# Optimization experiments

Measured on AMD Instinct MI355X. Metric: run time of the kernel, lower is better.

The kernel has to match this reference:

```python
import jax, jax.numpy as jnp
from jax import lax
import numpy as np

D_STATE = 16
D_CONV = 4
GROUPS = 4
TOKEN = 8


def group_norm(x, w, b, groups, eps=1e-5):
    # x: [B, C, H, W]; torch GroupNorm semantics
    B, C, H, W = x.shape
    xg = x.reshape(B, groups, C // groups, H, W)
    mu = xg.mean(axis=(2, 3, 4), keepdims=True)
    var = ((xg - mu) ** 2).mean(axis=(2, 3, 4), keepdims=True)
    xg = (xg - mu) / jnp.sqrt(var + eps)
    return xg.reshape(B, C, H, W) * w[None, :, None, None] + b[None, :, None, None]


def mamba_fwd(x, in_w, conv_w, conv_b, xproj_w, dt_w, dt_b, A_log, D, out_w):
    # x: [B, L, d_model]. Faithful mamba_ssm Mamba forward (no biases on in/out proj).
    Bsz, L, _ = x.shape
    d_inner = in_w.shape[0] // 2
    dt_rank = dt_w.shape[1]
    xz = x @ in_w.T                                   # [B, L, 2*d_inner]
    xi, z = jnp.split(xz, 2, axis=-1)
    # causal depthwise conv1d (kernel D_CONV) + SiLU
    xc = lax.conv_general_dilated(
        xi.transpose(0, 2, 1), conv_w, window_strides=(1,),
        padding=[(D_CONV - 1, 0)], dimension_numbers=("NCH", "OIH", "NCH"),
        feature_group_count=d_inner)
    xc = jax.nn.silu(xc + conv_b[None, :, None]).transpose(0, 2, 1)  # [B, L, d_inner]
    xdb = xc @ xproj_w.T                               # [B, L, dt_rank + 2*d_state]
    dt, Bm, Cm = jnp.split(xdb, [dt_rank, dt_rank + D_STATE], axis=-1)
    dt = jax.nn.softplus(dt @ dt_w.T + dt_b)           # [B, L, d_inner]
    A = -jnp.exp(A_log)                                # [d_inner, d_state]
    dA = jnp.exp(dt[..., None] * A)                    # [B, L, d_inner, d_state]
    dBx = dt[..., None] * Bm[:, :, None, :] * xc[..., None]

    def step(h, inp):
        dA_t, dBx_t, C_t = inp                         # [B,di,ds],[B,di,ds],[B,ds]
        h = dA_t * h + dBx_t
        y = jnp.einsum('bds,bs->bd', h, C_t)
        return h, y

    h0 = jnp.zeros((Bsz, d_inner, D_STATE), dtype=x.dtype)
    _, ys = lax.scan(step, h0, (dA.transpose(1, 0, 2, 3),
                                dBx.transpose(1, 0, 2, 3),
                                Cm.transpose(1, 0, 2)))
    y = ys.transpose(1, 0, 2) + xc * D                 # skip term D*x
    y = y * jax.nn.silu(z)
    return y @ out_w.T


def setup_inputs() -> dict:
    key = jax.random.key(0)
    ks = iter(jax.random.split(key, 48))

    def rn(shape, s=0.02):
        return jax.random.normal(next(ks), shape, dtype=jnp.float32) * s

    B, C, H, W = 4, 64, 64, 64
    inp = {"x": jax.random.normal(next(ks), (B, C, H, W), dtype=jnp.float32)}

    def mamba_params(prefix, d_model):
        d_inner = 2 * d_model
        dt_rank = -(-d_model // 16)
        inp[prefix + "_in_w"] = rn((2 * d_inner, d_model))
        inp[prefix + "_conv_w"] = rn((d_inner, 1, D_CONV))
        inp[prefix + "_conv_b"] = rn((d_inner,))
        inp[prefix + "_xproj_w"] = rn((dt_rank + 2 * D_STATE, d_inner))
        inp[prefix + "_dt_w"] = rn((d_inner, dt_rank))
        inp[prefix + "_dt_b"] = rn((d_inner,)) + 0.5
        inp[prefix + "_A_log"] = jnp.log(jnp.tile(jnp.arange(1, D_STATE + 1, dtype=jnp.float32), (d_inner, 1)))
        inp[prefix + "_D"] = jnp.ones((d_inner,), jnp.float32)
        inp[prefix + "_out_w"] = rn((d_model, d_inner))

    mamba_params("spa", C)
    mamba_params("spe", -(-C // TOKEN))  # group_channel_num = ceil(64/8) = 8
    inp["spa_gn_w"] = jnp.ones((C,), jnp.float32)
    inp["spa_gn_b"] = jnp.zeros((C,), jnp.float32)
    inp["spe_gn_w"] = jnp.ones((C,), jnp.float32)
    inp["spe_gn_b"] = jnp.zeros((C,), jnp.float32)
    inp["att_w"] = jnp.full((2,), 0.5, jnp.float32)
    return inp


def reference(x,
              spa_in_w, spa_conv_w, spa_conv_b, spa_xproj_w, spa_dt_w, spa_dt_b,
              spa_A_log, spa_D, spa_out_w,
              spe_in_w, spe_conv_w, spe_conv_b, spe_xproj_w, spe_dt_w, spe_dt_b,
              spe_A_log, spe_D, spe_out_w,
              spa_gn_w, spa_gn_b, spe_gn_w, spe_gn_b, att_w):
    B, C, H, W = x.shape
    gcn = -(-C // TOKEN)  # C == TOKEN*gcn here, so no padding path is taken

    # --- SpaMamba: flatten all pixels into one sequence [1, B*H*W, C] ---
    xs = x.transpose(0, 2, 3, 1).reshape(1, -1, C)
    ys = mamba_fwd(xs, spa_in_w, spa_conv_w, spa_conv_b, spa_xproj_w,
                   spa_dt_w, spa_dt_b, spa_A_log, spa_D, spa_out_w)
    ys = ys.reshape(B, H, W, C).transpose(0, 3, 1, 2)
    spa = jax.nn.silu(group_norm(ys, spa_gn_w, spa_gn_b, GROUPS)) + x

    # --- SpeMamba: per-pixel spectral tokens [B*H*W, TOKEN, gcn] ---
    xe = x.transpose(0, 2, 3, 1).reshape(B * H * W, TOKEN, gcn)
    ye = mamba_fwd(xe, spe_in_w, spe_conv_w, spe_conv_b, spe_xproj_w,
                   spe_dt_w, spe_dt_b, spe_A_log, spe_D, spe_out_w)
    ye = ye.reshape(B, H, W, C).transpose(0, 3, 1, 2)
    spe = x + jax.nn.silu(group_norm(ye, spe_gn_w, spe_gn_b, GROUPS))

    w = jax.nn.softmax(att_w)
    return spa * w[0] + spe * w[1] + x
```

## Files before the change

kernel.cpp:

```cpp
#include <hip/hip_runtime.h>

__device__ __forceinline__ float siluf(float x){ return x / (1.f + __expf(-x)); }
__device__ __forceinline__ float softplusf(float x){
    return fmaxf(x, 0.f) + __logf(1.f + __expf(-fabsf(x)));
}
#if __has_builtin(__builtin_amdgcn_exp2f)
__device__ __forceinline__ float fexp2(float x){ return __builtin_amdgcn_exp2f(x); }
#else
__device__ __forceinline__ float fexp2(float x){ return exp2f(x); }
#endif

__global__ void __launch_bounds__(256) k_xpose(const float* __restrict__ x, float* __restrict__ xs){
    __shared__ float t[64][65];
    int blk = blockIdx.x;
    int b = blk >> 6;
    int hw0 = (blk & 63) << 6;
    int tid = threadIdx.x;
    if (blk == 0 && tid < 192) xs[tid] = 0.f;
    const float* xb = x + b*262144 + hw0;
    #pragma unroll
    for (int it = 0; it < 16; ++it){
        int idx = it*256 + tid;
        t[idx>>6][idx&63] = xb[(idx>>6)*4096 + (idx&63)];
    }
    __syncthreads();
    float* xsb = xs + 192 + (size_t)(b*4096 + hw0)*64;
    #pragma unroll
    for (int it = 0; it < 16; ++it){
        int idx = it*256 + tid;
        xsb[(idx>>6)*64 + (idx&63)] = t[idx&63][idx>>6];
    }
}

__global__ void __launch_bounds__(256) k_inproj_conv(const float* __restrict__ xs,
        const float* __restrict__ in_w, const float* __restrict__ cw, const float* __restrict__ cb,
        float* __restrict__ xc, float* __restrict__ zb){
    int tid = threadIdx.x;
    int l0 = blockIdx.x * 8;
    float wr[64];
    const float4* w4 = (const float4*)(in_w + tid*64);
    #pragma unroll
    for (int k = 0; k < 16; ++k){
        float4 v = w4[k];
        wr[4*k]=v.x; wr[4*k+1]=v.y; wr[4*k+2]=v.z; wr[4*k+3]=v.w;
    }
    if (tid < 128){
        float acc[11];
        #pragma unroll
        for (int r = 0; r < 11; ++r) acc[r] = 0.f;
        const float4* xr = ((const float4*)xs) + (size_t)l0*16;
        #pragma unroll
        for (int k = 0; k < 16; ++k){
            #pragma unroll
            for (int r = 0; r < 11; ++r){
                float4 v = xr[r*16 + k];
                acc[r] = fmaf(v.x, wr[4*k],   acc[r]);
                acc[r] = fmaf(v.y, wr[4*k+1], acc[r]);
                acc[r] = fmaf(v.z, wr[4*k+2], acc[r]);
                acc[r] = fmaf(v.w, wr[4*k+3], acc[r]);
            }
        }
        float cw0 = cw[tid*4+0], cw1 = cw[tid*4+1], cw2 = cw[tid*4+2], cw3 = cw[tid*4+3];
        float cbd = cb[tid];
        #pragma unroll
        for (int r = 0; r < 8; ++r){
            float a = fmaf(cw0, acc[r],   cbd);
            a = fmaf(cw1, acc[r+1], a);
            a = fmaf(cw2, acc[r+2], a);
            a = fmaf(cw3, acc[r+3], a);
            xc[(size_t)(l0+r)*128 + tid] = siluf(a);
        }
    } else {
        float acc[8];
        #pragma unroll
        for (int r = 0; r < 8; ++r) acc[r] = 0.f;
        const float4* xr = ((const float4*)(xs + 192)) + (size_t)l0*16;
        #pragma unroll
        for (int k = 0; k < 16; ++k){
            #pragma unroll
            for (int r = 0; r < 8; ++r){
                float4 v = xr[r*16 + k];
                acc[r] = fmaf(v.x, wr[4*k],   acc[r]);
                acc[r] = fmaf(v.y, wr[4*k+1], acc[r]);
                acc[r] = fmaf(v.z, wr[4*k+2], acc[r]);
                acc[r] = fmaf(v.w, wr[4*k+3], acc[r]);
            }
        }
        int dz = tid - 128;
        #pragma unroll
        for (int r = 0; r < 8; ++r) zb[(size_t)(l0+r)*128 + dz] = acc[r];
    }
}

#define XE_  0
#define XCL_ 1216
#define BCL_ 3904
#define DTV_ 8640
#define SPG_ 8768
__global__ void __launch_bounds__(256) k_p1_spe(
        const float* __restrict__ xc, const float* __restrict__ xpw, const float* __restrict__ dtw,
        const float* __restrict__ dtb, const float* __restrict__ A_log,
        float* __restrict__ Pb, float* __restrict__ Qb,
        const float* __restrict__ x,
        const float* __restrict__ ein_w, const float* __restrict__ ecw, const float* __restrict__ ecb,
        const float* __restrict__ expw, const float* __restrict__ edtw, const float* __restrict__ edtb,
        const float* __restrict__ eA_log, const float* __restrict__ eDv, const float* __restrict__ eow,
        float* __restrict__ ye, float* __restrict__ sp)
{
    __shared__ float smem[8800];
    const int tid = threadIdx.x;
    if (blockIdx.x < 1024){
        float* sxc = smem;
        float* sbm = smem + 2048;
        float* dtr = smem + 2304;
        const int ch = blockIdx.x;
        {
            const float4* src = (const float4*)(xc + (size_t)ch*2048);
            float4* dst = (float4*)sxc;
            dst[tid] = src[tid];
            dst[256 + tid] = src[256 + tid];
        }
        __syncthreads();
        {
            int j = tid & 63, tg = tid >> 6;
            if (j < 20){
                const float4* w4  = (const float4*)(xpw + j*128);
                const float4* xc4 = (const float4*)sxc + tg*128;
                float acc[4];
                #pragma unroll
                for (int r = 0; r < 4; ++r) acc[r] = 0.f;
                #pragma unroll 8
                for (int k = 0; k < 32; ++k){
                    float4 w = w4[k];
                    #pragma unroll
                    for (int r = 0; r < 4; ++r){
                        float4 v = xc4[r*32 + k];
                        acc[r] = fmaf(v.x, w.x, acc[r]);
                        acc[r] = fmaf(v.y, w.y, acc[r]);
                        acc[r] = fmaf(v.z, w.z, acc[r]);
                        acc[r] = fmaf(v.w, w.w, acc[r]);
                    }
                }
                if (j < 4){
                    #pragma unroll
                    for (int r = 0; r < 4; ++r) dtr[(tg*4+r)*4 + j] = acc[r];
                } else {
                    #pragma unroll
                    for (int r = 0; r < 4; ++r) sbm[(tg*4+r)*16 + (j-4)] = acc[r];
                }
            }
        }
        __syncthreads();
        const int d  = tid & 127;
        const int sh = tid >> 7;
        float A8[8];
        {
            const float4* al4 = (const float4*)(A_log + d*16 + sh*8);
            float4 v0 = al4[0], v1 = al4[1];
            A8[0]=-__expf(v0.x)*1.44269504f; A8[1]=-__expf(v0.y)*1.44269504f;
            A8[2]=-__expf(v0.z)*1.44269504f; A8[3]=-__expf(v0.w)*1.44269504f;
            A8[4]=-__expf(v1.x)*1.44269504f; A8[5]=-__expf(v1.y)*1.44269504f;
            A8[6]=-__expf(v1.z)*1.44269504f; A8[7]=-__expf(v1.w)*1.44269504f;
        }
        float4 dw = *(const float4*)(dtw + d*4);
        float dbd = dtb[d];
        float P[8], Q[8];
        #pragma unroll
        for (int s = 0; s < 8; ++s){ P[s] = 1.f; Q[s] = 0.f; }
        #pragma unroll 4
        for (int i = 0; i < 16; ++i){
            float4 dt4 = *(const float4*)(dtr + i*4);
            float dv = dbd;
            dv = fmaf(dt4.x, dw.x, dv);
            dv = fmaf(dt4.y, dw.y, dv);
            dv = fmaf(dt4.z, dw.z, dv);
            dv = fmaf(dt4.w, dw.w, dv);
            float dt = softplusf(dv);
            float db = dt * sxc[i*128 + d];
            const float4* bmr = (const float4*)(sbm + i*16 + sh*8);
            float4 b0 = bmr[0], b1 = bmr[1];
            float bv[8] = {b0.x,b0.y,b0.z,b0.w,b1.x,b1.y,b1.z,b1.w};
            #pragma unroll
            for (int s = 0; s < 8; ++s){
                float a = fexp2(dt*A8[s]);
                P[s] *= a;
                Q[s] = fmaf(a, Q[s], db*bv[s]);
            }
        }
        float* Pp = Pb + (size_t)ch*2048 + d*16 + sh*8;
        float* Qp = Qb + (size_t)ch*2048 + d*16 + sh*8;
        ((float4*)Pp)[0] = make_float4(P[0],P[1],P[2],P[3]);
        ((float4*)Pp)[1] = make_float4(P[4],P[5],P[6],P[7]);
        ((float4*)Qp)[0] = make_float4(Q[0],Q[1],Q[2],Q[3]);
        ((float4*)Qp)[1] = make_float4(Q[4],Q[5],Q[6],Q[7]);
    } else {
        const int pix = tid >> 4;
        const int d   = tid & 15;
        const int eb  = blockIdx.x - 1024;
        const int p0  = eb * 16;
        const int b   = p0 >> 12;
        const int hw0 = p0 & 4095;

        const float* xb = x + b*262144 + hw0;
        #pragma unroll
        for (int it = 0; it < 4; ++it){
            int idx = it*256 + tid;
            smem[XE_ + (idx&15)*76 + (idx>>4)] = xb[(idx>>4)*4096 + (idx&15)];
        }
        __syncthreads();

        float wi[8], wz[8];
        #pragma unroll
        for (int g = 0; g < 8; ++g){ wi[g] = ein_w[d*8+g]; wz[g] = ein_w[(16+d)*8+g]; }
        float xi[8], zz[8];
        {
            const float4* xe4 = (const float4*)(smem + XE_ + pix*76);
            #pragma unroll
            for (int t = 0; t < 8; ++t){
                float4 a = xe4[t*2], bq = xe4[t*2+1];
                float xv8[8] = {a.x,a.y,a.z,a.w,bq.x,bq.y,bq.z,bq.w};
                float ai = 0.f, az = 0.f;
                #pragma unroll
                for (int g = 0; g < 8; ++g){
                    ai = fmaf(xv8[g], wi[g], ai);
                    az = fmaf(xv8[g], wz[g], az);
                }
                xi[t] = ai; zz[t] = az;
            }
        }
        float c0 = ecw[d*4+0], c1 = ecw[d*4+1], c2 = ecw[d*4+2], c3 = ecw[d*4+3];
        float cbd = ecb[d];
        float xcr[8];
        #pragma unroll
        for (int t = 0; t < 8; ++t){
            float a = fmaf(c3, xi[t], cbd);
            if (t >= 1) a = fmaf(c2, xi[t-1], a);
            if (t >= 2) a = fmaf(c1, xi[t-2], a);
            if (t >= 3) a = fmaf(c0, xi[t-3], a);
            xcr[t] = siluf(a);
            smem[XCL_ + pix*168 + t*20 + d] = xcr[t];
        }
        __syncthreads();

        {
            const int row = tid >> 1;
            const int jh  = tid & 1;
            const int px2 = row >> 3;
            const int t2  = row & 7;
            const float4* xr = (const float4*)(smem + XCL_ + px2*168 + t2*20);
            float4 r0 = xr[0], r1 = xr[1], r2 = xr[2], r3 = xr[3];
            float xv[16] = {r0.x,r0.y,r0.z,r0.w, r1.x,r1.y,r1.z,r1.w,
                            r2.x,r2.y,r2.z,r2.w, r3.x,r3.y,r3.z,r3.w};
            float accd = 0.f;
            #pragma unroll
            for (int k = 0; k < 16; ++k) accd = fmaf(xv[k], expw[k], accd);
            const float* wbase = expw + (1 + jh*16)*16;
            float outv[16];
            #pragma unroll
            for (int s = 0; s < 16; ++s){
                const float* wr = wbase + s*16;
                float a = 0.f;
                #pragma unroll
                for (int k = 0; k < 16; ++k) a = fmaf(xv[k], wr[k], a);
                outv[s] = a;
            }
            float* dstb = smem + BCL_ + px2*296 + t2*36 + jh*16;
            #pragma unroll
            for (int s = 0; s < 16; ++s) dstb[s] = outv[s];
            if (jh == 0) smem[DTV_ + px2*8 + t2] = accd;
        }
        __syncthreads();

        float A16[16];
        #pragma unroll
        for (int s = 0; s < 16; ++s) A16[s] = -__expf(eA_log[d*16+s]) * 1.44269504f;
        float dwd = edtw[d], dbd = edtb[d], Dd = eDv[d];
        float h[16];
        #pragma unroll
        for (int s = 0; s < 16; ++s) h[s] = 0.f;
        #pragma unroll
        for (int t = 0; t < 8; ++t){
            float dtd = softplusf(fmaf(smem[DTV_ + pix*8 + t], dwd, dbd));
            float db = dtd * xcr[t];
            const float4* bc4 = (const float4*)(smem + BCL_ + pix*296 + t*36);
            float4 b0 = bc4[0], b1 = bc4[1], b2 = bc4[2], b3 = bc4[3];
            float4 cc0 = bc4[4], cc1 = bc4[5], cc2 = bc4[6], cc3 = bc4[7];
            float bv[16] = {b0.x,b0.y,b0.z,b0.w, b1.x,b1.y,b1.z,b1.w,
                            b2.x,b2.y,b2.z,b2.w, b3.x,b3.y,b3.z,b3.w};
            float cv[16] = {cc0.x,cc0.y,cc0.z,cc0.w, cc1.x,cc1.y,cc1.z,cc1.w,
                            cc2.x,cc2.y,cc2.z,cc2.w, cc3.x,cc3.y,cc3.z,cc3.w};
            float yp = 0.f;
            #pragma unroll
            for (int s = 0; s < 16; ++s){
                float a = fexp2(dtd*A16[s]);
                h[s] = fmaf(a, h[s], db*bv[s]);
                yp = fmaf(h[s], cv[s], yp);
            }
            smem[pix*168 + t*20 + d] = (yp + xcr[t]*Dd) * siluf(zz[t]);
        }
        __syncthreads();

        int tt = d >> 1, m0 = (d & 1)*4;
        const float4* y4 = (const float4*)(smem + pix*168 + tt*20);
        float4 y0 = y4[0], y1 = y4[1], y2 = y4[2], y3 = y4[3];
        float ylr[16] = {y0.x,y0.y,y0.z,y0.w, y1.x,y1.y,y1.z,y1.w,
                         y2.x,y2.y,y2.z,y2.w, y3.x,y3.y,y3.z,y3.w};
        float acc[4];
        #pragma unroll
        for (int mm = 0; mm < 4; ++mm){
            const float* wr = eow + (m0+mm)*16;
            float a = 0.f;
            #pragma unroll
            for (int k = 0; k < 16; ++k) a = fmaf(ylr[k], wr[k], a);
            acc[mm] = a;
        }
        float4 o; o.x=acc[0]; o.y=acc[1]; o.z=acc[2]; o.w=acc[3];
        *(float4*)(ye + (size_t)(p0+pix)*64 + tt*8 + m0) = o;

        float s  = acc[0]+acc[1]+acc[2]+acc[3];
        float ss = acc[0]*acc[0]+acc[1]*acc[1]+acc[2]*acc[2]+acc[3]*acc[3];
        s += __shfl_xor(s,1);  ss += __shfl_xor(ss,1);
        s += __shfl_xor(s,2);  ss += __shfl_xor(ss,2);
        s += __shfl_xor(s,16); ss += __shfl_xor(ss,16);
        s += __shfl_xor(s,32); ss += __shfl_xor(ss,32);
        int lane = tid & 63, wv = tid >> 6;
        if ((lane & 51) == 0){ smem[SPG_ + wv*4 + ((lane>>2)&3)] = s; smem[SPG_ + 16 + wv*4 + ((lane>>2)&3)] = ss; }
        __syncthreads();
        if (tid < 4){
            int blk = eb & 255;
            float S  = smem[SPG_+0*4+tid]+smem[SPG_+1*4+tid]+smem[SPG_+2*4+tid]+smem[SPG_+3*4+tid];
            float SS = smem[SPG_+16+0*4+tid]+smem[SPG_+16+1*4+tid]+smem[SPG_+16+2*4+tid]+smem[SPG_+16+3*4+tid];
            float* dst = sp + (size_t)(((4 + b)*4 + tid)*512 + blk*2);
            dst[0] = S; dst[1] = SS;
        }
    }
}

__global__ void __launch_bounds__(256) k_scan_p2a(const float* __restrict__ Pb,
        const float* __restrict__ Qb, float* __restrict__ Ps, float* __restrict__ Qs){
    int g = blockIdx.x*256 + threadIdx.x;
    int sup = g >> 11;
    int lane = g & 2047;
    float P = 1.f, Q = 0.f;
    for (int i = 0; i < 64; i += 8){
        float p[8], q[8];
        #pragma unroll
        for (int u = 0; u < 8; ++u){
            p[u] = Pb[(size_t)(sup*64+i+u)*2048 + lane];
            q[u] = Qb[(size_t)(sup*64+i+u)*2048 + lane];
        }
        #pragma unroll
        for (int u = 0; u < 8; ++u){
            P = p[u]*P;
            Q = fmaf(p[u], Q, q[u]);
        }
    }
    Ps[g] = P; Qs[g] = Q;
}

__global__ void __launch_bounds__(256) k_scan_p2c(const float* __restrict__ Pb,
        const float* __restrict__ Qb, const float* __restrict__ Ps,
        const float* __restrict__ Qs, float* __restrict__ Hs){
    int g = blockIdx.x*256 + threadIdx.x;
    int sup = g >> 11;
    int lane = g & 2047;
    float h = 0.f;
    for (int u = 0; u < sup; ++u){
        float p = Ps[u*2048 + lane];
        float q = Qs[u*2048 + lane];
        h = fmaf(p, h, q);
    }
    for (int i = 0; i < 64; i += 8){
        float p[8], q[8];
        #pragma unroll
        for (int u = 0; u < 8; ++u){
            p[u] = Pb[(size_t)(sup*64+i+u)*2048 + lane];
            q[u] = Qb[(size_t)(sup*64+i+u)*2048 + lane];
        }
        #pragma unroll
        for (int u = 0; u < 8; ++u){
            Hs[(size_t)(sup*64+i+u)*2048 + lane] = h;
            h = fmaf(p[u], h, q[u]);
        }
    }
}

__global__ void __launch_bounds__(256) k_scan_p3(const float* __restrict__ xc,
        const float* __restrict__ zb, const float* __restrict__ xpw, const float* __restrict__ dtw,
        const float* __restrict__ dtb, const float* __restrict__ A_log, const float* __restrict__ Dv,
        const float* __restrict__ Hs, const float* __restrict__ ow,
        float* __restrict__ ys, float* __restrict__ sp){
    __shared__ float sxc[16*128];
    __shared__ float ypl[2][16*128];
    __shared__ float sbm[16*16];
    __shared__ float scm[16*16];
    __shared__ __align__(16) float dtr[16][4];
    __shared__ float pgs[2][2][4];
    const int tid = threadIdx.x;
    const int ch = blockIdx.x;
    {
        const float4* src = (const float4*)(xc + (size_t)ch*2048);
        float4* dst = (float4*)sxc;
        dst[tid] = src[tid];
        dst[256 + tid] = src[256 + tid];
    }
    __syncthreads();
    {
        int j = tid & 63, tg = tid >> 6;
        if (j < 36){
            const float4* w4  = (const float4*)(xpw + j*128);
            const float4* xc4 = (const float4*)sxc + tg*128;
            float acc[4];
            #pragma unroll
            for (int r = 0; r < 4; ++r) acc[r] = 0.f;
            #pragma unroll 8
            for (int k = 0; k < 32; ++k){
                float4 w = w4[k];
                #pragma unroll
                for (int r = 0; r < 4; ++r){
                    float4 v = xc4[r*32 + k];
                    acc[r] = fmaf(v.x, w.x, acc[r]);
                    acc[r] = fmaf(v.y, w.y, acc[r]);
                    acc[r] = fmaf(v.z, w.z, acc[r]);
                    acc[r] = fmaf(v.w, w.w, acc[r]);
                }
            }
            if (j < 4){
                #pragma unroll
                for (int r = 0; r < 4; ++r) dtr[tg*4+r][j] = acc[r];
            } else if (j < 20){
                #pragma unroll
                for (int r = 0; r < 4; ++r) sbm[(tg*4+r)*16 + (j-4)] = acc[r];
            } else {
                #pragma unroll
                for (int r = 0; r < 4; ++r) scm[(tg*4+r)*16 + (j-20)] = acc[r];
            }
        }
    }
    __syncthreads();
    const int d  = tid & 127;
    const int sh = tid >> 7;
    float A8[8], h[8];
    {
        const float4* al4 = (const float4*)(A_log + d*16 + sh*8);
        float4 v0 = al4[0], v1 = al4[1];
        A8[0]=-__expf(v0.x)*1.44269504f; A8[1]=-__expf(v0.y)*1.44269504f;
        A8[2]=-__expf(v0.z)*1.44269504f; A8[3]=-__expf(v0.w)*1.44269504f;
        A8[4]=-__expf(v1.x)*1.44269504f; A8[5]=-__expf(v1.y)*1.44269504f;
        A8[6]=-__expf(v1.z)*1.44269504f; A8[7]=-__expf(v1.w)*1.44269504f;
        const float4* h4 = (const float4*)(Hs + (size_t)ch*2048 + d*16 + sh*8);
        float4 h0 = h4[0], h1 = h4[1];
        h[0]=h0.x; h[1]=h0.y; h[2]=h0.z; h[3]=h0.w;
        h[4]=h1.x; h[5]=h1.y; h[6]=h1.z; h[7]=h1.w;
    }
    float4 dw = *(const float4*)(dtw + d*4);
    float dbd = dtb[d];
    #pragma unroll 4
    for (int i = 0; i < 16; ++i){
        float4 dt4 = *(const float4*)dtr[i];
        float dv = dbd;
        dv = fmaf(dt4.x, dw.x, dv);
        dv = fmaf(dt4.y, dw.y, dv);
        dv = fmaf(dt4.z, dw.z, dv);
        dv = fmaf(dt4.w, dw.w, dv);
        float dt = softplusf(dv);
        float db = dt * sxc[i*128 + d];
        const float4* bmr = (const float4*)(sbm + i*16 + sh*8);
        const float4* cmr = (const float4*)(scm + i*16 + sh*8);
        float4 b0 = bmr[0], b1 = bmr[1];
        float4 c0 = cmr[0], c1 = cmr[1];
        float bv[8] = {b0.x,b0.y,b0.z,b0.w,b1.x,b1.y,b1.z,b1.w};
        float cv[8] = {c0.x,c0.y,c0.z,c0.w,c1.x,c1.y,c1.z,c1.w};
        float yp = 0.f;
        #pragma unroll
        for (int s = 0; s < 8; ++s){
            float a = fexp2(dt*A8[s]);
            h[s] = fmaf(a, h[s], db*bv[s]);
            yp = fmaf(h[s], cv[s], yp);
        }
        ypl[sh][i*128 + d] = yp;
    }
    __syncthreads();
    #pragma unroll
    for (int it = 0; it < 8; ++it){
        int idx = it*256 + tid;
        float yp = ypl[0][idx] + ypl[1][idx];
        float xcd = sxc[idx];
        float zv = zb[(size_t)ch*2048 + idx];
        ypl[0][idx] = (yp + xcd*Dv[idx & 127]) * siluf(zv);
    }
    __syncthreads();
    {
        int c  = tid & 63;
        int kh = (tid >> 6) & 1;
        int rg = tid >> 7;
        float wr[64];
        const float4* w4o = (const float4*)(ow + c*128 + kh*64);
        #pragma unroll
        for (int k = 0; k < 16; ++k){
            float4 v = w4o[k];
            wr[4*k]=v.x; wr[4*k+1]=v.y; wr[4*k+2]=v.z; wr[4*k+3]=v.w;
        }
        float acc[8];
        #pragma unroll
        for (int r = 0; r < 8; ++r) acc[r] = 0.f;
        const float4* y4 = (const float4*)(ypl[0] + rg*8*128 + kh*64);
        #pragma unroll
        for (int k = 0; k < 16; ++k){
            #pragma unroll
            for (int r = 0; r < 8; ++r){
                float4 v = y4[r*32 + k];
                acc[r] = fmaf(v.x, wr[4*k],   acc[r]);
                acc[r] = fmaf(v.y, wr[4*k+1], acc[r]);
                acc[r] = fmaf(v.z, wr[4*k+2], acc[r]);
                acc[r] = fmaf(v.w, wr[4*k+3], acc[r]);
            }
        }
        float* part = ypl[1];
        if (kh == 1){
            #pragma unroll
            for (int r = 0; r < 8; ++r) part[(rg*8+r)*64 + c] = acc[r];
        }
        __syncthreads();
        if (kh == 0){
            float s = 0.f, ss = 0.f;
            #pragma unroll
            for (int r = 0; r < 8; ++r){
                float v = acc[r] + part[(rg*8+r)*64 + c];
                ys[(size_t)(ch*16 + rg*8 + r)*64 + c] = v;
                s += v; ss += v*v;
            }
            s += __shfl_xor(s,1); ss += __shfl_xor(ss,1);
            s += __shfl_xor(s,2); ss += __shfl_xor(ss,2);
            s += __shfl_xor(s,4); ss += __shfl_xor(ss,4);
            s += __shfl_xor(s,8); ss += __shfl_xor(ss,8);
            if ((c & 15) == 0){ pgs[0][rg][c>>4] = s; pgs[1][rg][c>>4] = ss; }
        }
        __syncthreads();
        if (tid < 4){
            int b = ch >> 8, blk = ch & 255;
            float S  = pgs[0][0][tid] + pgs[0][1][tid];
            float SS = pgs[1][0][tid] + pgs[1][1][tid];
            float* dst = sp + (size_t)((b*4 + tid)*512 + blk*2);
            dst[0] = S; dst[1] = SS;
        }
    }
}

__global__ void __launch_bounds__(256) k_final(const float* __restrict__ x,
        const float* __restrict__ ys, const float* __restrict__ ye,
        const float* __restrict__ sp,
        const float* __restrict__ gsw, const float* __restrict__ gsb,
        const float* __restrict__ gew, const float* __restrict__ geb,
        const float* __restrict__ attw, float* __restrict__ out){
    __shared__ float st[16];
    __shared__ float tys[32][65];
    __shared__ float tye[32][65];
    int tid = threadIdx.x;
    int b   = blockIdx.x >> 7;
    int hw0 = (blockIdx.x & 127) << 5;
    {
        int combo = tid >> 5;
        int j = tid & 31;
        int t = combo >> 2, g = combo & 3;
        const float4* bp = (const float4*)(sp + (size_t)(t*16 + b*4 + g)*512 + j*16);
        float s = 0.f, ss = 0.f;
        #pragma unroll
        for (int k = 0; k < 4; ++k){ float4 v = bp[k]; s += v.x+v.z; ss += v.y+v.w; }
        s += __shfl_xor(s,1);  ss += __shfl_xor(ss,1);
        s += __shfl_xor(s,2);  ss += __shfl_xor(ss,2);
        s += __shfl_xor(s,4);  ss += __shfl_xor(ss,4);
        s += __shfl_xor(s,8);  ss += __shfl_xor(ss,8);
        s += __shfl_xor(s,16); ss += __shfl_xor(ss,16);
        if (j == 0){
            float m = s * (1.f/65536.f);
            float v = ss * (1.f/65536.f) - m*m;
            st[combo*2]   = m;
            st[combo*2+1] = rsqrtf(v + 1e-5f);
        }
    }
    const float* ysb = ys + ((size_t)(b*4096 + hw0))*64;
    const float* yeb = ye + ((size_t)(b*4096 + hw0))*64;
    #pragma unroll
    for (int it = 0; it < 8; ++it){
        int idx = it*256 + tid;
        tys[idx>>6][idx&63] = ysb[idx];
        tye[idx>>6][idx&63] = yeb[idx];
    }
    __syncthreads();
    float a0 = attw[0], a1 = attw[1];
    float mx = fmaxf(a0, a1);
    float e0 = __expf(a0-mx), e1 = __expf(a1-mx);
    float inv = 1.f/(e0+e1);
    float w0 = e0*inv, w1 = e1*inv;
    #pragma unroll
    for (int it = 0; it < 8; ++it){
        int idx = it*256 + tid;
        int c = idx >> 5, hwi = idx & 31;
        int g = c >> 4;
        size_t gx = ((size_t)(b*64 + c))*4096 + hw0 + hwi;
        float xv = x[gx];
        float ns = (tys[hwi][c] - st[g*2])     * st[g*2+1]     * gsw[c] + gsb[c];
        float ne = (tye[hwi][c] - st[8+g*2])   * st[8+g*2+1]   * gew[c] + geb[c];
        out[gx] = w0*(siluf(ns)+xv) + w1*(xv+siluf(ne)) + xv;
    }
}

#define OFF_XS 0u
#define OFF_XC 1048832u
#define OFF_Z  3145984u
#define OFF_PB 5243136u
#define OFF_QB 7340288u
#define OFF_HS 9437440u
#define OFF_YE 11534592u
#define OFF_PS 12583168u
#define OFF_QS 12615936u
#define OFF_SP 12648704u

extern "C" void kernel_launch(void* const* d_in, const int* in_sizes, int n_in,
                              void* d_out, int out_size, void* d_ws, size_t ws_size,
                              hipStream_t stream) {
    const float* x           = (const float*)d_in[0];
    const float* spa_in_w    = (const float*)d_in[1];
    const float* spa_conv_w  = (const float*)d_in[2];
    const float* spa_conv_b  = (const float*)d_in[3];
    const float* spa_xproj_w = (const float*)d_in[4];
    const float* spa_dt_w    = (const float*)d_in[5];
    const float* spa_dt_b    = (const float*)d_in[6];
    const float* spa_A_log   = (const float*)d_in[7];
    const float* spa_D       = (const float*)d_in[8];
    const float* spa_out_w   = (const float*)d_in[9];
    const float* spe_in_w    = (const float*)d_in[10];
    const float* spe_conv_w  = (const float*)d_in[11];
    const float* spe_conv_b  = (const float*)d_in[12];
    const float* spe_xproj_w = (const float*)d_in[13];
    const float* spe_dt_w    = (const float*)d_in[14];
    const float* spe_dt_b    = (const float*)d_in[15];
    const float* spe_A_log   = (const float*)d_in[16];
    const float* spe_D       = (const float*)d_in[17];
    const float* spe_out_w   = (const float*)d_in[18];
    const float* spa_gn_w    = (const float*)d_in[19];
    const float* spa_gn_b    = (const float*)d_in[20];
    const float* spe_gn_w    = (const float*)d_in[21];
    const float* spe_gn_b    = (const float*)d_in[22];
    const float* att_w       = (const float*)d_in[23];

    float* ws  = (float*)d_ws;
    float* xs  = ws + OFF_XS;
    float* xc  = ws + OFF_XC;
    float* zb  = ws + OFF_Z;
    float* Pb  = ws + OFF_PB;
    float* Qb  = ws + OFF_QB;
    float* Hs  = ws + OFF_HS;
    float* Ps  = ws + OFF_PS;
    float* Qs  = ws + OFF_QS;
    float* sp  = ws + OFF_SP;
    float* ysb = ws + OFF_XS;
    float* yeb = ws + OFF_YE;
    float* out = (float*)d_out;

    k_xpose      <<<256,  256, 0, stream>>>(x, xs);
    k_inproj_conv<<<2048, 256, 0, stream>>>(xs, spa_in_w, spa_conv_w, spa_conv_b, xc, zb);
    k_p1_spe     <<<2048, 256, 0, stream>>>(xc, spa_xproj_w, spa_dt_w, spa_dt_b, spa_A_log,
                                            Pb, Qb,
                                            x, spe_in_w, spe_conv_w, spe_conv_b, spe_xproj_w,
                                            spe_dt_w, spe_dt_b, spe_A_log, spe_D, spe_out_w,
                                            yeb, sp);
    k_scan_p2a   <<<128,  256, 0, stream>>>(Pb, Qb, Ps, Qs);
    k_scan_p2c   <<<128,  256, 0, stream>>>(Pb, Qb, Ps, Qs, Hs);
    k_scan_p3    <<<1024, 256, 0, stream>>>(xc, zb, spa_xproj_w, spa_dt_w, spa_dt_b,
                                            spa_A_log, spa_D, Hs, spa_out_w, ysb, sp);
    k_final      <<<512,  256, 0, stream>>>(x, ysb, yeb, sp, spa_gn_w, spa_gn_b,
                                            spe_gn_w, spe_gn_b, att_w, out);
}
```

Baseline: 123.5 us.

## Split fused spatial-scan/spectral kernel into two launches and remap spectral thread layout

Separates the heterogeneous k_p1_spe kernel, which branched on blockIdx between spatial scan phase-1 and the spectral Mamba path, into two dedicated kernels, k_scan_p1 and k_spe. Each kernel can then get its own register and shared-memory allocation instead of sharing the worst case of both branches. In k_spe, the x_proj B/C work is remapped so each half-block handles one half of the outputs, with float4 stores to shared memory. The out-proj lane mapping and shuffle reduction pattern change to match. The trade-off is an extra launch and the loss of concurrency between the two workloads within one grid.

```diff
diff --git a/kernel.cpp b/kernel.cpp
--- a/kernel.cpp
+++ b/kernel.cpp
@@ -92,15 +92,101 @@
     }
 }
 
+__global__ void __launch_bounds__(256) k_scan_p1(const float* __restrict__ xc,
+        const float* __restrict__ xpw, const float* __restrict__ dtw, const float* __restrict__ dtb,
+        const float* __restrict__ A_log, float* __restrict__ Pb, float* __restrict__ Qb){
+    __shared__ float sxc[2048];
+    __shared__ float sbm[256];
+    __shared__ __align__(16) float dtr[64];
+    const int tid = threadIdx.x;
+    const int ch = blockIdx.x;
+    {
+        const float4* src = (const float4*)(xc + (size_t)ch*2048);
+        float4* dst = (float4*)sxc;
+        dst[tid] = src[tid];
+        dst[256 + tid] = src[256 + tid];
+    }
+    __syncthreads();
+    {
+        int j = tid & 63, tg = tid >> 6;
+        if (j < 20){
+            const float4* w4  = (const float4*)(xpw + j*128);
+            const float4* xc4 = (const float4*)sxc + tg*128;
+            float acc[4];
+            #pragma unroll
+            for (int r = 0; r < 4; ++r) acc[r] = 0.f;
+            #pragma unroll 8
+            for (int k = 0; k < 32; ++k){
+                float4 w = w4[k];
+                #pragma unroll
+                for (int r = 0; r < 4; ++r){
+                    float4 v = xc4[r*32 + k];
+                    acc[r] = fmaf(v.x, w.x, acc[r]);
+                    acc[r] = fmaf(v.y, w.y, acc[r]);
+                    acc[r] = fmaf(v.z, w.z, acc[r]);
+                    acc[r] = fmaf(v.w, w.w, acc[r]);
+                }
+            }
+            if (j < 4){
+                #pragma unroll
+                for (int r = 0; r < 4; ++r) dtr[(tg*4+r)*4 + j] = acc[r];
+            } else {
+                #pragma unroll
+                for (int r = 0; r < 4; ++r) sbm[(tg*4+r)*16 + (j-4)] = acc[r];
+            }
+        }
+    }
+    __syncthreads();
+    const int d  = tid & 127;
+    const int sh = tid >> 7;
+    float A8[8];
+    {
+        const float4* al4 = (const float4*)(A_log + d*16 + sh*8);
+        float4 v0 = al4[0], v1 = al4[1];
+        A8[0]=-__expf(v0.x)*1.44269504f; A8[1]=-__expf(v0.y)*1.44269504f;
+        A8[2]=-__expf(v0.z)*1.44269504f; A8[3]=-__expf(v0.w)*1.44269504f;
+        A8[4]=-__expf(v1.x)*1.44269504f; A8[5]=-__expf(v1.y)*1.44269504f;
+        A8[6]=-__expf(v1.z)*1.44269504f; A8[7]=-__expf(v1.w)*1.44269504f;
+    }
+    float4 dw = *(const float4*)(dtw + d*4);
+    float dbd = dtb[d];
+    float P[8], Q[8];
+    #pragma unroll
+    for (int s = 0; s < 8; ++s){ P[s] = 1.f; Q[s] = 0.f; }
+    #pragma unroll 4
+    for (int i = 0; i < 16; ++i){
+        float4 dt4 = *(const float4*)(dtr + i*4);
+        float dv = dbd;
+        dv = fmaf(dt4.x, dw.x, dv);
+        dv = fmaf(dt4.y, dw.y, dv);
+        dv = fmaf(dt4.z, dw.z, dv);
+        dv = fmaf(dt4.w, dw.w, dv);
+        float dt = softplusf(dv);
+        float db = dt * sxc[i*128 + d];
+        const float4* bmr = (const float4*)(sbm + i*16 + sh*8);
+        float4 b0 = bmr[0], b1 = bmr[1];
+        float bv[8] = {b0.x,b0.y,b0.z,b0.w,b1.x,b1.y,b1.z,b1.w};
+        #pragma unroll
+        for (int s = 0; s < 8; ++s){
+            float a = fexp2(dt*A8[s]);
+            P[s] *= a;
+            Q[s] = fmaf(a, Q[s], db*bv[s]);
+        }
+    }
+    float* Pp = Pb + (size_t)ch*2048 + d*16 + sh*8;
+    float* Qp = Qb + (size_t)ch*2048 + d*16 + sh*8;
+    ((float4*)Pp)[0] = make_float4(P[0],P[1],P[2],P[3]);
+    ((float4*)Pp)[1] = make_float4(P[4],P[5],P[6],P[7]);
+    ((float4*)Qp)[0] = make_float4(Q[0],Q[1],Q[2],Q[3]);
+    ((float4*)Qp)[1] = make_float4(Q[4],Q[5],Q[6],Q[7]);
+}
+
 #define XE_  0
 #define XCL_ 1216
 #define BCL_ 3904
 #define DTV_ 8640
 #define SPG_ 8768
-__global__ void __launch_bounds__(256) k_p1_spe(
-        const float* __restrict__ xc, const float* __restrict__ xpw, const float* __restrict__ dtw,
-        const float* __restrict__ dtb, const float* __restrict__ A_log,
-        float* __restrict__ Pb, float* __restrict__ Qb,
+__global__ void __launch_bounds__(256) k_spe(
         const float* __restrict__ x,
         const float* __restrict__ ein_w, const float* __restrict__ ecw, const float* __restrict__ ecb,
         const float* __restrict__ expw, const float* __restrict__ edtw, const float* __restrict__ edtb,
@@ -109,199 +195,123 @@
 {
     __shared__ float smem[8800];
     const int tid = threadIdx.x;
-    if (blockIdx.x < 1024){
-        float* sxc = smem;
-        float* sbm = smem + 2048;
-        float* dtr = smem + 2304;
-        const int ch = blockIdx.x;
-        {
-            const float4* src = (const float4*)(xc + (size_t)ch*2048);
-            float4* dst = (float4*)sxc;
-            dst[tid] = src[tid];
-            dst[256 + tid] = src[256 + tid];
-        }
-        __syncthreads();
-        {
-            int j = tid & 63, tg = tid >> 6;
-            if (j < 20){
-                const float4* w4  = (const float4*)(xpw + j*128);
-                const float4* xc4 = (const float4*)sxc + tg*128;
-                float acc[4];
-                #pragma unroll
-                for (int r = 0; r < 4; ++r) acc[r] = 0.f;
-                #pragma unroll 8
-                for (int k = 0; k < 32; ++k){
-                    float4 w = w4[k];
-                    #pragma unroll
-                    for (int r = 0; r < 4; ++r){
-                        float4 v = xc4[r*32 + k];
-                        acc[r] = fmaf(v.x, w.x, acc[r]);
-                        acc[r] = fmaf(v.y, w.y, acc[r]);
-                        acc[r] = fmaf(v.z, w.z, acc[r]);
-                        acc[r] = fmaf(v.w, w.w, acc[r]);
-                    }
-                }
-                if (j < 4){
-                    #pragma unroll
-                    for (int r = 0; r < 4; ++r) dtr[(tg*4+r)*4 + j] = acc[r];
-                } else {
-                    #pragma unroll
-                    for (int r = 0; r < 4; ++r) sbm[(tg*4+r)*16 + (j-4)] = acc[r];
-                }
-            }
-        }
-        __syncthreads();
-        const int d  = tid & 127;
-        const int sh = tid >> 7;
-        float A8[8];
-        {
-            const float4* al4 = (const float4*)(A_log + d*16 + sh*8);
-            float4 v0 = al4[0], v1 = al4[1];
-            A8[0]=-__expf(v0.x)*1.44269504f; A8[1]=-__expf(v0.y)*1.44269504f;
-            A8[2]=-__expf(v0.z)*1.44269504f; A8[3]=-__expf(v0.w)*1.44269504f;
-            A8[4]=-__expf(v1.x)*1.44269504f; A8[5]=-__expf(v1.y)*1.44269504f;
-            A8[6]=-__expf(v1.z)*1.44269504f; A8[7]=-__expf(v1.w)*1.44269504f;
-        }
-        float4 dw = *(const float4*)(dtw + d*4);
-        float dbd = dtb[d];
-        float P[8], Q[8];
-        #pragma unroll
-        for (int s = 0; s < 8; ++s){ P[s] = 1.f; Q[s] = 0.f; }
-        #pragma unroll 4
-        for (int i = 0; i < 16; ++i){
-            float4 dt4 = *(const float4*)(dtr + i*4);
-            float dv = dbd;
-            dv = fmaf(dt4.x, dw.x, dv);
-            dv = fmaf(dt4.y, dw.y, dv);
-            dv = fmaf(dt4.z, dw.z, dv);
-            dv = fmaf(dt4.w, dw.w, dv);
-            float dt = softplusf(dv);
-            float db = dt * sxc[i*128 + d];
-            const float4* bmr = (const float4*)(sbm + i*16 + sh*8);
-            float4 b0 = bmr[0], b1 = bmr[1];
-            float bv[8] = {b0.x,b0.y,b0.z,b0.w,b1.x,b1.y,b1.z,b1.w};
-            #pragma unroll
-            for (int s = 0; s < 8; ++s){
-                float a = fexp2(dt*A8[s]);
-                P[s] *= a;
-                Q[s] = fmaf(a, Q[s], db*bv[s]);
-            }
-        }
-        float* Pp = Pb + (size_t)ch*2048 + d*16 + sh*8;
-        float* Qp = Qb + (size_t)ch*2048 + d*16 + sh*8;
-        ((float4*)Pp)[0] = make_float4(P[0],P[1],P[2],P[3]);
-        ((float4*)Pp)[1] = make_float4(P[4],P[5],P[6],P[7]);
-        ((float4*)Qp)[0] = make_float4(Q[0],Q[1],Q[2],Q[3]);
-        ((float4*)Qp)[1] = make_float4(Q[4],Q[5],Q[6],Q[7]);
-    } else {
-        const int pix = tid >> 4;
-        const int d   = tid & 15;
-        const int eb  = blockIdx.x - 1024;
-        const int p0  = eb * 16;
-        const int b   = p0 >> 12;
-        const int hw0 = p0 & 4095;
-
-        const float* xb = x + b*262144 + hw0;
-        #pragma unroll
-        for (int it = 0; it < 4; ++it){
-            int idx = it*256 + tid;
-            smem[XE_ + (idx&15)*76 + (idx>>4)] = xb[(idx>>4)*4096 + (idx&15)];
-        }
-        __syncthreads();
-
-        float wi[8], wz[8];
-        #pragma unroll
-        for (int g = 0; g < 8; ++g){ wi[g] = ein_w[d*8+g]; wz[g] = ein_w[(16+d)*8+g]; }
-        float xi[8], zz[8];
-        {
-            const float4* xe4 = (const float4*)(smem + XE_ + pix*76);
-            #pragma unroll
-            for (int t = 0; t < 8; ++t){
-                float4 a = xe4[t*2], bq = xe4[t*2+1];
-                float xv8[8] = {a.x,a.y,a.z,a.w,bq.x,bq.y,bq.z,bq.w};
-                float ai = 0.f, az = 0.f;
-                #pragma unroll
-                for (int g = 0; g < 8; ++g){
-                    ai = fmaf(xv8[g], wi[g], ai);
-                    az = fmaf(xv8[g], wz[g], az);
-                }
-                xi[t] = ai; zz[t] = az;
-            }
-        }
-        float c0 = ecw[d*4+0], c1 = ecw[d*4+1], c2 = ecw[d*4+2], c3 = ecw[d*4+3];
-        float cbd = ecb[d];
-        float xcr[8];
+    const int pix = tid >> 4;
+    const int d   = tid & 15;
+    const int eb  = blockIdx.x;
+    const int p0  = eb * 16;
+    const int b   = p0 >> 12;
+    const int hw0 = p0 & 4095;
+
+    const float* xb = x + b*262144 + hw0;
+    #pragma unroll
+    for (int it = 0; it < 4; ++it){
+        int idx = it*256 + tid;
+        smem[XE_ + (idx&15)*76 + (idx>>4)] = xb[(idx>>4)*4096 + (idx&15)];
+    }
+    __syncthreads();
+
+    float wi[8], wz[8];
+    #pragma unroll
+    for (int g = 0; g < 8; ++g){ wi[g] = ein_w[d*8+g]; wz[g] = ein_w[(16+d)*8+g]; }
+    float xi[8], zz[8];
+    {
+        const float4* xe4 = (const float4*)(smem + XE_ + pix*76);
         #pragma unroll
         for (int t = 0; t < 8; ++t){
-            float a = fmaf(c3, xi[t], cbd);
-            if (t >= 1) a = fmaf(c2, xi[t-1], a);
-            if (t >= 2) a = fmaf(c1, xi[t-2], a);
-            if (t >= 3) a = fmaf(c0, xi[t-3], a);
-            xcr[t] = siluf(a);
-            smem[XCL_ + pix*168 + t*20 + d] = xcr[t];
-        }
-        __syncthreads();
-
-        {
-            const int row = tid >> 1;
-            const int jh  = tid & 1;
-            const int px2 = row >> 3;
-            const int t2  = row & 7;
-            const float4* xr = (const float4*)(smem + XCL_ + px2*168 + t2*20);
-            float4 r0 = xr[0], r1 = xr[1], r2 = xr[2], r3 = xr[3];
-            float xv[16] = {r0.x,r0.y,r0.z,r0.w, r1.x,r1.y,r1.z,r1.w,
-                            r2.x,r2.y,r2.z,r2.w, r3.x,r3.y,r3.z,r3.w};
+            float4 a = xe4[t*2], bq = xe4[t*2+1];
+            float xv8[8] = {a.x,a.y,a.z,a.w,bq.x,bq.y,bq.z,bq.w};
+            float ai = 0.f, az = 0.f;
+            #pragma unroll
+            for (int g = 0; g < 8; ++g){
+                ai = fmaf(xv8[g], wi[g], ai);
+                az = fmaf(xv8[g], wz[g], az);
+            }
+            xi[t] = ai; zz[t] = az;
+        }
+    }
+    float c0 = ecw[d*4+0], c1 = ecw[d*4+1], c2 = ecw[d*4+2], c3 = ecw[d*4+3];
+    float cbd = ecb[d];
+    float xcr[8];
+    #pragma unroll
+    for (int t = 0; t < 8; ++t){
+        float a = fmaf(c3, xi[t], cbd);
+        if (t >= 1) a = fmaf(c2, xi[t-1], a);
+        if (t >= 2) a = fmaf(c1, xi[t-2], a);
+        if (t >= 3) a = fmaf(c0, xi[t-3], a);
+        xcr[t] = siluf(a);
+        smem[XCL_ + pix*168 + t*20 + d] = xcr[t];
+    }
+    __syncthreads();
+
+    {
+        const int row = tid & 127;
+        const int jh  = tid >> 7;
+        const int px2 = row >> 3;
+        const int t2  = row & 7;
+        const float4* xr = (const float4*)(smem + XCL_ + px2*168 + t2*20);
+        float4 r0 = xr[0], r1 = xr[1], r2 = xr[2], r3 = xr[3];
+        float xv[16] = {r0.x,r0.y,r0.z,r0.w, r1.x,r1.y,r1.z,r1.w,
+                        r2.x,r2.y,r2.z,r2.w, r3.x,r3.y,r3.z,r3.w};
+        const float* wbase = expw + (1 + jh*16)*16;
+        float outv[16];
+        #pragma unroll
+        for (int s = 0; s < 16; ++s){
+            const float* wr = wbase + s*16;
+            float a = 0.f;
+            #pragma unroll
+            for (int k = 0; k < 16; ++k) a = fmaf(xv[k], wr[k], a);
+            outv[s] = a;
+        }
+        float4* dst4 = (float4*)(smem + BCL_ + px2*296 + t2*36 + jh*16);
+        dst4[0] = make_float4(outv[0], outv[1], outv[2], outv[3]);
+        dst4[1] = make_float4(outv[4], outv[5], outv[6], outv[7]);
+        dst4[2] = make_float4(outv[8], outv[9], outv[10],outv[11]);
+        dst4[3] = make_float4(outv[12],outv[13],outv[14],outv[15]);
+        if (jh == 0){
             float accd = 0.f;
             #pragma unroll
             for (int k = 0; k < 16; ++k) accd = fmaf(xv[k], expw[k], accd);
-            const float* wbase = expw + (1 + jh*16)*16;
-            float outv[16];
-            #pragma unroll
-            for (int s = 0; s < 16; ++s){
-                const float* wr = wbase + s*16;
-                float a = 0.f;
-                #pragma unroll
-                for (int k = 0; k < 16; ++k) a = fmaf(xv[k], wr[k], a);
-                outv[s] = a;
-            }
-            float* dstb = smem + BCL_ + px2*296 + t2*36 + jh*16;
-            #pragma unroll
-            for (int s = 0; s < 16; ++s) dstb[s] = outv[s];
-            if (jh == 0) smem[DTV_ + px2*8 + t2] = accd;
-        }
-        __syncthreads();
-
-        float A16[16];
-        #pragma unroll
-        for (int s = 0; s < 16; ++s) A16[s] = -__expf(eA_log[d*16+s]) * 1.44269504f;
-        float dwd = edtw[d], dbd = edtb[d], Dd = eDv[d];
-        float h[16];
-        #pragma unroll
-        for (int s = 0; s < 16; ++s) h[s] = 0.f;
-        #pragma unroll
-        for (int t = 0; t < 8; ++t){
-            float dtd = softplusf(fmaf(smem[DTV_ + pix*8 + t], dwd, dbd));
-            float db = dtd * xcr[t];
-            const float4* bc4 = (const float4*)(smem + BCL_ + pix*296 + t*36);
-            float4 b0 = bc4[0], b1 = bc4[1], b2 = bc4[2], b3 = bc4[3];
-            float4 cc0 = bc4[4], cc1 = bc4[5], cc2 = bc4[6], cc3 = bc4[7];
-            float bv[16] = {b0.x,b0.y,b0.z,b0.w, b1.x,b1.y,b1.z,b1.w,
-                            b2.x,b2.y,b2.z,b2.w, b3.x,b3.y,b3.z,b3.w};
-            float cv[16] = {cc0.x,cc0.y,cc0.z,cc0.w, cc1.x,cc1.y,cc1.z,cc1.w,
-                            cc2.x,cc2.y,cc2.z,cc2.w, cc3.x,cc3.y,cc3.z,cc3.w};
-            float yp = 0.f;
-            #pragma unroll
-            for (int s = 0; s < 16; ++s){
-                float a = fexp2(dtd*A16[s]);
-                h[s] = fmaf(a, h[s], db*bv[s]);
-                yp = fmaf(h[s], cv[s], yp);
-            }
-            smem[pix*168 + t*20 + d] = (yp + xcr[t]*Dd) * siluf(zz[t]);
-        }
-        __syncthreads();
-
-        int tt = d >> 1, m0 = (d & 1)*4;
-        const float4* y4 = (const float4*)(smem + pix*168 + tt*20);
+            smem[DTV_ + px2*8 + t2] = accd;
+        }
+    }
+    __syncthreads();
+
+    float A16[16];
+    #pragma unroll
+    for (int s = 0; s < 16; ++s) A16[s] = -__expf(eA_log[d*16+s]) * 1.44269504f;
+    float dwd = edtw[d], dbd = edtb[d], Dd = eDv[d];
+    float h[16];
+    #pragma unroll
+    for (int s = 0; s < 16; ++s) h[s] = 0.f;
+    #pragma unroll
+    for (int t = 0; t < 8; ++t){
+        float dtd = softplusf(fmaf(smem[DTV_ + pix*8 + t], dwd, dbd));
+        float db = dtd * xcr[t];
+        const float4* bc4 = (const float4*)(smem + BCL_ + pix*296 + t*36);
+        float4 b0 = bc4[0], b1 = bc4[1], b2 = bc4[2], b3 = bc4[3];
+        float4 cc0 = bc4[4], cc1 = bc4[5], cc2 = bc4[6], cc3 = bc4[7];
+        float bv[16] = {b0.x,b0.y,b0.z,b0.w, b1.x,b1.y,b1.z,b1.w,
+                        b2.x,b2.y,b2.z,b2.w, b3.x,b3.y,b3.z,b3.w};
+        float cv[16] = {cc0.x,cc0.y,cc0.z,cc0.w, cc1.x,cc1.y,cc1.z,cc1.w,
+                        cc2.x,cc2.y,cc2.z,cc2.w, cc3.x,cc3.y,cc3.z,cc3.w};
+        float yp = 0.f;
+        #pragma unroll
+        for (int s = 0; s < 16; ++s){
+            float a = fexp2(dtd*A16[s]);
+            h[s] = fmaf(a, h[s], db*bv[s]);
+            yp = fmaf(h[s], cv[s], yp);
+        }
+        smem[pix*168 + t*20 + d] = (yp + xcr[t]*Dd) * siluf(zz[t]);
+    }
+    __syncthreads();
+
+    {
+        const int half = tid >> 7;
+        const int idx7 = tid & 127;
+        const int pixD = idx7 >> 3;
+        const int ttD  = idx7 & 7;
+        const int m0   = half*4;
+        const float4* y4 = (const float4*)(smem + pixD*168 + ttD*20);
         float4 y0 = y4[0], y1 = y4[1], y2 = y4[2], y3 = y4[3];
         float ylr[16] = {y0.x,y0.y,y0.z,y0.w, y1.x,y1.y,y1.z,y1.w,
                          y2.x,y2.y,y2.z,y2.w, y3.x,y3.y,y3.z,y3.w};
@@ -315,24 +325,27 @@
             acc[mm] = a;
         }
         float4 o; o.x=acc[0]; o.y=acc[1]; o.z=acc[2]; o.w=acc[3];
-        *(float4*)(ye + (size_t)(p0+pix)*64 + tt*8 + m0) = o;
+        *(float4*)(ye + (size_t)(p0+pixD)*64 + ttD*8 + m0) = o;
 
         float s  = acc[0]+acc[1]+acc[2]+acc[3];
         float ss = acc[0]*acc[0]+acc[1]*acc[1]+acc[2]*acc[2]+acc[3]*acc[3];
         s += __shfl_xor(s,1);  ss += __shfl_xor(ss,1);
-        s += __shfl_xor(s,2);  ss += __shfl_xor(ss,2);
+        s += __shfl_xor(s,8);  ss += __shfl_xor(ss,8);
         s += __shfl_xor(s,16); ss += __shfl_xor(ss,16);
         s += __shfl_xor(s,32); ss += __shfl_xor(ss,32);
         int lane = tid & 63, wv = tid >> 6;
-        if ((lane & 51) == 0){ smem[SPG_ + wv*4 + ((lane>>2)&3)] = s; smem[SPG_ + 16 + wv*4 + ((lane>>2)&3)] = ss; }
-        __syncthreads();
-        if (tid < 4){
-            int blk = eb & 255;
-            float S  = smem[SPG_+0*4+tid]+smem[SPG_+1*4+tid]+smem[SPG_+2*4+tid]+smem[SPG_+3*4+tid];
-            float SS = smem[SPG_+16+0*4+tid]+smem[SPG_+16+1*4+tid]+smem[SPG_+16+2*4+tid]+smem[SPG_+16+3*4+tid];
-            float* dst = sp + (size_t)(((4 + b)*4 + tid)*512 + blk*2);
-            dst[0] = S; dst[1] = SS;
-        }
+        if ((lane & 57) == 0){
+            smem[SPG_ + wv*4 + ((lane>>1)&3)] = s;
+            smem[SPG_ + 16 + wv*4 + ((lane>>1)&3)] = ss;
+        }
+    }
+    __syncthreads();
+    if (tid < 4){
+        int blk = eb & 255;
+        float S  = smem[SPG_+0*4+tid]+smem[SPG_+1*4+tid]+smem[SPG_+2*4+tid]+smem[SPG_+3*4+tid];
+        float SS = smem[SPG_+16+0*4+tid]+smem[SPG_+16+1*4+tid]+smem[SPG_+16+2*4+tid]+smem[SPG_+16+3*4+tid];
+        float* dst = sp + (size_t)(((4 + b)*4 + tid)*512 + blk*2);
+        dst[0] = S; dst[1] = SS;
     }
 }
 
@@ -661,9 +674,9 @@
 
     k_xpose      <<<256,  256, 0, stream>>>(x, xs);
     k_inproj_conv<<<2048, 256, 0, stream>>>(xs, spa_in_w, spa_conv_w, spa_conv_b, xc, zb);
-    k_p1_spe     <<<2048, 256, 0, stream>>>(xc, spa_xproj_w, spa_dt_w, spa_dt_b, spa_A_log,
-                                            Pb, Qb,
-                                            x, spe_in_w, spe_conv_w, spe_conv_b, spe_xproj_w,
+    k_scan_p1    <<<1024, 256, 0, stream>>>(xc, spa_xproj_w, spa_dt_w, spa_dt_b, spa_A_log,
+                                            Pb, Qb);
+    k_spe        <<<1024, 256, 0, stream>>>(x, spe_in_w, spe_conv_w, spe_conv_b, spe_xproj_w,
                                             spe_dt_w, spe_dt_b, spe_A_log, spe_D, spe_out_w,
                                             yeb, sp);
     k_scan_p2a   <<<128,  256, 0, stream>>>(Pb, Qb, Ps, Qs);
```

Measured after the change: 120.4 us. 1.03x faster.
